# Performance work log

Measured on AMD Instinct MI355X. Metric: run time of the kernel, lower is better.

Reference implementation:

```python
import jax, jax.numpy as jnp
import numpy as np

RADIUS = 0.2
NSAMPLE = 32

B, N, S, C = 4, 16384, 4096, 64


def _ball_query(xyz, new_xyz):
    """CUDA ball_query semantics: for each centroid, the first NSAMPLE point
    indices with squared distance < radius^2 (in index order); empty slots are
    filled with the first found index (0 if no neighbor).
    xyz: [B,N,3], new_xyz: [B,S,3] -> idx [B,S,NSAMPLE] int32."""
    n = xyz.shape[1]
    # squared pairwise distances [B,S,N] via |a|^2 + |b|^2 - 2 a.b
    d2 = (jnp.sum(new_xyz * new_xyz, -1)[:, :, None]
          + jnp.sum(xyz * xyz, -1)[:, None, :]
          - 2.0 * jnp.einsum('bsd,bnd->bsn', new_xyz, xyz))
    in_ball = d2 < RADIUS * RADIUS
    # key = point index if in ball else N (sentinel); sorting gives first-K order
    key = jnp.where(in_ball, jnp.arange(n, dtype=jnp.int32), jnp.int32(n))
    key = jnp.sort(key, axis=-1)[..., :NSAMPLE]          # [B,S,K]
    first = key[..., :1]
    first = jnp.where(first == n, 0, first)              # no neighbor -> 0
    idx = jnp.where(key == n, first, key)
    return idx


def _group(feat, idx):
    """feat [B,C,N], idx [B,S,K] -> [B,C,S,K] (group_points_forward)."""
    return jax.vmap(lambda f, i: f[:, i])(feat, idx)


def setup_inputs() -> dict:
    key = jax.random.key(0)
    k1, k2, k3 = jax.random.split(key, 3)
    xyz = jax.random.uniform(k1, (B, N, 3), dtype=jnp.float32)
    new_xyz = jax.random.uniform(k2, (B, S, 3), dtype=jnp.float32)
    features = jax.random.normal(k3, (B, C, N), dtype=jnp.float32)
    return {"xyz": xyz, "new_xyz": new_xyz, "features": features}


def reference(xyz, new_xyz, features):
    idx = jax.lax.stop_gradient(_ball_query(xyz, new_xyz))   # [B,S,K], non-diff
    xyz_t = jnp.transpose(xyz, (0, 2, 1))                    # [B,3,N]
    grouped_xyz = _group(xyz_t, idx)                         # [B,3,S,K]
    grouped_xyz = grouped_xyz - jnp.transpose(new_xyz, (0, 2, 1))[..., None]
    grouped_features = _group(features, idx)                 # [B,C,S,K]
    new_features = jnp.concatenate([grouped_xyz, grouped_features], axis=1)
    return new_features                                      # [B,3+C,S,K]
```

## Files before the change

### kernel.cpp

```cpp
#include <hip/hip_runtime.h>
#include <stdint.h>

#define BB 4
#define NN 16384
#define SS 4096
#define CC 64
#define KK 32

#define T_INT    10736108
#define LOW_INT  10709108
#define BAND_W   54000

#define PACKED_BYTES ((size_t)BB * NN * sizeof(float4))
#define IDX_BYTES    ((size_t)BB * SS * KK * sizeof(int))

typedef short short2v __attribute__((ext_vector_type(2)));

static __device__ __forceinline__ int mbcnt64(unsigned long long m) {
    return (int)__builtin_amdgcn_mbcnt_hi((unsigned)(m >> 32),
               __builtin_amdgcn_mbcnt_lo((unsigned)m, 0u));
}

#if __has_builtin(__builtin_amdgcn_sdot2)
static __device__ __forceinline__ int dot2i(short2v a, short2v b, int c) {
    return __builtin_amdgcn_sdot2(a, b, c, false);
}
#else
static __device__ __forceinline__ int dot2i(short2v a, short2v b, int c) {
    return (int)a.x * (int)b.x + (int)a.y * (int)b.y + c;
}
#endif

static __device__ __forceinline__ unsigned short f2bf(float f) {
    unsigned u = __builtin_bit_cast(unsigned, f);
    return (unsigned short)((u + 0x7FFFu + ((u >> 16) & 1u)) >> 16);
}
static __device__ __forceinline__ float bf_lo(unsigned w) {
    return __builtin_bit_cast(float, w << 16);
}
static __device__ __forceinline__ float bf_hi(unsigned w) {
    return __builtin_bit_cast(float, w & 0xFFFF0000u);
}

__global__ __launch_bounds__(256) void prep_kernel(const float* __restrict__ xyz,
                                                   const float* __restrict__ features,
                                                   float4* __restrict__ packed,
                                                   ushort4* __restrict__ qpts,
                                                   unsigned short* __restrict__ featB) {
    int blk = blockIdx.x;
    if (blk < 64) {
        for (int i = 0; i < 4; ++i) {
            int p = blk * 1024 + i * 256 + (int)threadIdx.x;
            float x = xyz[(size_t)p * 3 + 0];
            float y = xyz[(size_t)p * 3 + 1];
            float z = xyz[(size_t)p * 3 + 2];
            packed[p] = make_float4(x, y, z, 0.0f);
            ushort4 q;
            q.x = (unsigned short)rintf(x * 16383.0f);
            q.y = (unsigned short)rintf(y * 16383.0f);
            q.z = (unsigned short)rintf(z * 16383.0f);
            q.w = 0;
            qpts[p] = q;
        }
        return;
    }
    blk -= 64;
    int b  = blk >> 8;
    int n0 = (blk & 255) << 6;
    const float* f = features + (size_t)b * CC * NN;
    for (int i = 0; i < 4; ++i) {
        int e  = (int)threadIdx.x + i * 256;
        int c4 = e & 15;
        int n  = n0 + (e >> 4);
        ushort4 v;
        v.x = f2bf(f[(size_t)(c4 * 4 + 0) * NN + n]);
        v.y = f2bf(f[(size_t)(c4 * 4 + 1) * NN + n]);
        v.z = f2bf(f[(size_t)(c4 * 4 + 2) * NN + n]);
        v.w = f2bf(f[(size_t)(c4 * 4 + 3) * NN + n]);
        *(ushort4*)(featB + ((size_t)b * NN + n) * 64 + c4 * 4) = v;
    }
}

__global__ __launch_bounds__(256) void fused_kernel(const float4* __restrict__ packed,
                                                    const ushort4* __restrict__ qpts,
                                                    const float* __restrict__ new_xyz,
                                                    const unsigned short* __restrict__ featB,
                                                    float* __restrict__ out) {
    __shared__ int   sidx[128];
    __shared__ float snc[12];
    __shared__ uint4 sfeat[64][8];

    int bid  = (int)blockIdx.x;
    int wgid = (bid & 7) * 512 + (bid >> 3);
    int b  = wgid >> 10;
    int s0 = (wgid & 1023) << 2;
    int t  = (int)threadIdx.x;
    int w = t >> 6, lane = t & 63;
    int s = s0 + w;

    if (t < 12) snc[t] = new_xyz[((size_t)(b * SS + s0 + t / 3)) * 3 + (t % 3)];

    const float* nc = new_xyz + (size_t)(b * SS + s) * 3;
    const float nxf = nc[0], nyf = nc[1], nzf = nc[2];
    const int qcx = (int)rintf(nxf * 16383.0f);
    const int qcy = (int)rintf(nyf * 16383.0f);
    const int qcz = (int)rintf(nzf * 16383.0f);
    const short2v cxy2 = __builtin_bit_cast(short2v, (unsigned)((qcy << 16) | (qcx & 0xFFFF)));
    const short2v cz2  = __builtin_bit_cast(short2v, (unsigned)qcz);
    const double nx = (double)nxf, ny = (double)nyf, nz = (double)nzf;
    const double t1 = nx * nx + ny * ny + nz * nz;
    const double r2 = 0.2 * 0.2;

    const float4* pts = packed + (size_t)b * NN;
    const uint4*  qv  = (const uint4*)(qpts + (size_t)b * NN);

#define TESTQ(WXY, WZ, J, INB)                                                  \
    {                                                                           \
        short2v dxy = __builtin_bit_cast(short2v, (WXY)) - cxy2;                \
        short2v dz2 = __builtin_bit_cast(short2v, (WZ))  - cz2;                 \
        int d2i = dot2i(dxy, dxy, dot2i(dz2, dz2, 0));                          \
        if ((unsigned)(d2i - LOW_INT) < (unsigned)BAND_W) {                     \
            float4 p = pts[J];                                                  \
            double pxd = (double)p.x, pyd = (double)p.y, pzd = (double)p.z;     \
            double t2d = pxd * pxd + pyd * pyd + pzd * pzd;                     \
            double dtd = nx * pxd + ny * pyd + nz * pzd;                        \
            INB = ((t1 + t2d) - 2.0 * dtd) < r2;                                \
        } else {                                                                \
            INB = d2i < T_INT;                                                  \
        }                                                                       \
    }

    int cnt = 0;
    int first = 0;
    uint4 u0 = qv[lane];
    uint4 u1 = qv[64 + lane];
    for (int i = 0; i < NN / 2; i += 128) {
        int nb = (i + 128 < NN / 2) ? (i + 128) : i;
        uint4 n0 = qv[nb + lane];
        uint4 n1 = qv[nb + 64 + lane];
        int base = i * 2;
        int jA = base + 2 * lane;
        int jC = base + 128 + 2 * lane;

        bool iA, iB, iC, iD;
        TESTQ(u0.x, u0.y, jA, iA)
        TESTQ(u0.z, u0.w, jA + 1, iB)
        TESTQ(u1.x, u1.y, jC, iC)
        TESTQ(u1.z, u1.w, jC + 1, iD)

        unsigned long long mA = __ballot(iA);
        unsigned long long mB = __ballot(iB);
        unsigned long long mC = __ballot(iC);
        unsigned long long mD = __ballot(iD);

        if (cnt == 0 && (mA | mB | mC | mD)) {
            if (mA | mB) {
                int cA = mA ? 2 * (int)__builtin_ctzll(mA)     : 0x7FFFFFFF;
                int cB = mB ? 2 * (int)__builtin_ctzll(mB) + 1 : 0x7FFFFFFF;
                first = base + (cA < cB ? cA : cB);
            } else {
                int cC = mC ? 2 * (int)__builtin_ctzll(mC)     : 0x7FFFFFFF;
                int cD = mD ? 2 * (int)__builtin_ctzll(mD) + 1 : 0x7FFFFFFF;
                first = base + 128 + (cC < cD ? cC : cD);
            }
        }
        int preAB = mbcnt64(mA) + mbcnt64(mB);
        int cAB   = (int)__popcll(mA) + (int)__popcll(mB);
        int preCD = mbcnt64(mC) + mbcnt64(mD);
        if (iA) { int sl = cnt + preAB;                      if (sl < KK) sidx[w * KK + sl] = jA; }
        if (iB) { int sl = cnt + preAB + (iA ? 1 : 0);       if (sl < KK) sidx[w * KK + sl] = jA + 1; }
        if (iC) { int sl = cnt + cAB + preCD;                if (sl < KK) sidx[w * KK + sl] = jC; }
        if (iD) { int sl = cnt + cAB + preCD + (iC ? 1 : 0); if (sl < KK) sidx[w * KK + sl] = jC + 1; }
        cnt += cAB + (int)__popcll(mC) + (int)__popcll(mD);
        if (cnt >= KK) break;
        u0 = n0; u1 = n1;
    }
#undef TESTQ
    if (lane >= cnt && lane < KK) sidx[w * KK + lane] = first;
    __syncthreads();

    const size_t cs = (size_t)SS * KK;
    size_t obase = (size_t)(b * 67) * cs + (size_t)s0 * KK;
    if (t < 128) {
        int cl = t >> 5, k = t & 31;
        float4 p = pts[sidx[t]];
        size_t o = obase + (size_t)cl * KK + k;
        out[o]          = p.x - snc[cl * 3 + 0];
        out[o + cs]     = p.y - snc[cl * 3 + 1];
        out[o + 2 * cs] = p.z - snc[cl * 3 + 2];
    }

    for (int pass = 0; pass < 2; ++pass) {
        {
            int rl = t >> 2;
            int q  = t & 3;
            const uint4* src = (const uint4*)(featB +
                ((size_t)b * NN + sidx[pass * 64 + rl]) * 64);
            sfeat[rl][(q * 2     + rl) & 7] = src[q * 2];
            sfeat[rl][(q * 2 + 1 + rl) & 7] = src[q * 2 + 1];
        }
        __syncthreads();

        float* pbase = out + obase + (size_t)pass * 64;
        for (int cc = 0; cc < 2; ++cc) {
            int c8 = w * 2 + cc;
            uint4 v = sfeat[lane][(c8 + lane) & 7];
            float* pl = pbase + lane;
            size_t cb = (size_t)(3 + c8 * 8) * cs;
            pl[cb]          = bf_lo(v.x);
            pl[cb + cs]     = bf_hi(v.x);
            pl[cb + 2 * cs] = bf_lo(v.y);
            pl[cb + 3 * cs] = bf_hi(v.y);
            pl[cb + 4 * cs] = bf_lo(v.z);
            pl[cb + 5 * cs] = bf_hi(v.z);
            pl[cb + 6 * cs] = bf_lo(v.w);
            pl[cb + 7 * cs] = bf_hi(v.w);
        }
        __syncthreads();
    }
}

extern "C" void kernel_launch(void* const* d_in, const int* in_sizes, int n_in,
                              void* d_out, int out_size, void* d_ws, size_t ws_size,
                              hipStream_t stream) {
    const float* xyz      = (const float*)d_in[0];
    const float* new_xyz  = (const float*)d_in[1];
    const float* features = (const float*)d_in[2];
    float* out = (float*)d_out;

    float4*         packed = (float4*)d_ws;
    ushort4*        qpts   = (ushort4*)((char*)d_ws + PACKED_BYTES);
    unsigned short* featB  = (unsigned short*)((char*)d_ws + PACKED_BYTES + IDX_BYTES);

    prep_kernel<<<64 + BB * (NN / 64), 256, 0, stream>>>(xyz, features, packed,
                                                         qpts, featB);
    fused_kernel<<<BB * SS / 4, 256, 0, stream>>>(packed, qpts, new_xyz, featB, out);
}
```

Baseline: 45.76 us.

## Make gather/scatter phase wave-local to remove block-wide barriers

Each wave now gathers and writes out its own centroid's 32 neighbors, using a per-wave shared-memory slice, instead of the block cooperatively handling all four centroids in two passes. This removes the three __syncthreads barriers and the shared centroid-coordinate staging, so waves that finish the ball query early can start writing without waiting for the rest of the block. In exchange, output stores become 32-float segments per wave rather than 64/128-float contiguous runs, which may reduce write coalescing. The code also relies on wavefront-synchronous access to shared memory with no explicit wave barrier.

```diff
diff --git a/kernel.cpp b/kernel.cpp
--- a/kernel.cpp
+++ b/kernel.cpp
@@ -87,8 +87,7 @@
                                                     const unsigned short* __restrict__ featB,
                                                     float* __restrict__ out) {
     __shared__ int   sidx[128];
-    __shared__ float snc[12];
-    __shared__ uint4 sfeat[64][8];
+    __shared__ uint4 sfeat[4][32][8];
 
     int bid  = (int)blockIdx.x;
     int wgid = (bid & 7) * 512 + (bid >> 3);
@@ -97,8 +96,6 @@
     int t  = (int)threadIdx.x;
     int w = t >> 6, lane = t & 63;
     int s = s0 + w;
-
-    if (t < 12) snc[t] = new_xyz[((size_t)(b * SS + s0 + t / 3)) * 3 + (t % 3)];
 
     const float* nc = new_xyz + (size_t)(b * SS + s) * 3;
     const float nxf = nc[0], nyf = nc[1], nzf = nc[2];
@@ -177,46 +174,42 @@
     }
 #undef TESTQ
     if (lane >= cnt && lane < KK) sidx[w * KK + lane] = first;
-    __syncthreads();
 
     const size_t cs = (size_t)SS * KK;
-    size_t obase = (size_t)(b * 67) * cs + (size_t)s0 * KK;
-    if (t < 128) {
-        int cl = t >> 5, k = t & 31;
-        float4 p = pts[sidx[t]];
-        size_t o = obase + (size_t)cl * KK + k;
-        out[o]          = p.x - snc[cl * 3 + 0];
-        out[o + cs]     = p.y - snc[cl * 3 + 1];
-        out[o + 2 * cs] = p.z - snc[cl * 3 + 2];
-    }
-
-    for (int pass = 0; pass < 2; ++pass) {
-        {
-            int rl = t >> 2;
-            int q  = t & 3;
-            const uint4* src = (const uint4*)(featB +
-                ((size_t)b * NN + sidx[pass * 64 + rl]) * 64);
-            sfeat[rl][(q * 2     + rl) & 7] = src[q * 2];
-            sfeat[rl][(q * 2 + 1 + rl) & 7] = src[q * 2 + 1];
-        }
-        __syncthreads();
-
-        float* pbase = out + obase + (size_t)pass * 64;
-        for (int cc = 0; cc < 2; ++cc) {
-            int c8 = w * 2 + cc;
-            uint4 v = sfeat[lane][(c8 + lane) & 7];
-            float* pl = pbase + lane;
-            size_t cb = (size_t)(3 + c8 * 8) * cs;
-            pl[cb]          = bf_lo(v.x);
-            pl[cb + cs]     = bf_hi(v.x);
-            pl[cb + 2 * cs] = bf_lo(v.y);
-            pl[cb + 3 * cs] = bf_hi(v.y);
-            pl[cb + 4 * cs] = bf_lo(v.z);
-            pl[cb + 5 * cs] = bf_hi(v.z);
-            pl[cb + 6 * cs] = bf_lo(v.w);
-            pl[cb + 7 * cs] = bf_hi(v.w);
-        }
-        __syncthreads();
+    size_t obase = (size_t)(b * 67) * cs + (size_t)s * KK;
+
+    if (lane < KK) {
+        float4 p = pts[sidx[w * KK + lane]];
+        size_t o = obase + lane;
+        out[o]          = p.x - nxf;
+        out[o + cs]     = p.y - nyf;
+        out[o + 2 * cs] = p.z - nzf;
+    }
+
+    {
+        int row = lane >> 1;
+        int q   = lane & 1;
+        const uint4* src = (const uint4*)(featB +
+            ((size_t)b * NN + sidx[w * KK + row]) * 64) + q * 4;
+#pragma unroll
+        for (int j = 0; j < 4; ++j)
+            sfeat[w][row][(q * 4 + j + row) & 7] = src[j];
+    }
+
+#pragma unroll
+    for (int i = 0; i < 4; ++i) {
+        int k  = lane & 31;
+        int c8 = i * 2 + (lane >> 5);
+        uint4 v = sfeat[w][k][(c8 + k) & 7];
+        float* pl = out + obase + (size_t)(3 + c8 * 8) * cs + k;
+        pl[0]               = bf_lo(v.x);
+        pl[cs]              = bf_hi(v.x);
+        pl[2 * cs]          = bf_lo(v.y);
+        pl[3 * cs]          = bf_hi(v.y);
+        pl[4 * cs]          = bf_lo(v.z);
+        pl[5 * cs]          = bf_hi(v.z);
+        pl[6 * cs]          = bf_lo(v.w);
+        pl[7 * cs]          = bf_hi(v.w);
     }
 }
 
```

After: 45.90 us. About the same (+0.3%).

## Process sixteen centroids per block and gather all feature rows in one pass

Applied to the files above, without the earlier changes.

Each workgroup now loops over four groups of four centroids, so the grid shrinks from 4096 to 1024 blocks. The feature gather loads all 128 neighbour rows into a larger shared buffer in a single pass, with four uint4 loads per thread. The two-pass loop and one barrier per group are removed. This is meant to amortise per-block setup and barrier cost, but it cuts the number of resident waves and may reduce latency hiding on the irregular ball-query search.

```diff
diff --git a/kernel.cpp b/kernel.cpp
--- a/kernel.cpp
+++ b/kernel.cpp
@@ -88,37 +88,42 @@
                                                     float* __restrict__ out) {
     __shared__ int   sidx[128];
     __shared__ float snc[12];
-    __shared__ uint4 sfeat[64][8];
+    __shared__ uint4 sfeat[128][8];
 
     int bid  = (int)blockIdx.x;
-    int wgid = (bid & 7) * 512 + (bid >> 3);
-    int b  = wgid >> 10;
-    int s0 = (wgid & 1023) << 2;
+    int wgid = (bid & 7) * 128 + (bid >> 3);
+    int b     = wgid >> 8;
+    int sbase = (wgid & 255) << 4;
     int t  = (int)threadIdx.x;
     int w = t >> 6, lane = t & 63;
-    int s = s0 + w;
-
-    if (t < 12) snc[t] = new_xyz[((size_t)(b * SS + s0 + t / 3)) * 3 + (t % 3)];
-
-    const float* nc = new_xyz + (size_t)(b * SS + s) * 3;
-    const float nxf = nc[0], nyf = nc[1], nzf = nc[2];
-    const int qcx = (int)rintf(nxf * 16383.0f);
-    const int qcy = (int)rintf(nyf * 16383.0f);
-    const int qcz = (int)rintf(nzf * 16383.0f);
-    const short2v cxy2 = __builtin_bit_cast(short2v, (unsigned)((qcy << 16) | (qcx & 0xFFFF)));
-    const short2v cz2  = __builtin_bit_cast(short2v, (unsigned)qcz);
-    const double nx = (double)nxf, ny = (double)nyf, nz = (double)nzf;
-    const double t1 = nx * nx + ny * ny + nz * nz;
-    const double r2 = 0.2 * 0.2;
 
     const float4* pts = packed + (size_t)b * NN;
     const uint4*  qv  = (const uint4*)(qpts + (size_t)b * NN);
+    const size_t cs = (size_t)SS * KK;
+
+    for (int g = 0; g < 4; ++g) {
+        int s0 = sbase + g * 4;
+        int s  = s0 + w;
+
+        if (t < 12) snc[t] = new_xyz[((size_t)(b * SS + s0 + t / 3)) * 3 + (t % 3)];
+
+        const float* nc = new_xyz + (size_t)(b * SS + s) * 3;
+        const float nxf = nc[0], nyf = nc[1], nzf = nc[2];
+        const int qcx = (int)rintf(nxf * 16383.0f);
+        const int qcy = (int)rintf(nyf * 16383.0f);
+        const int qcz = (int)rintf(nzf * 16383.0f);
+        const short2v cxy2 = __builtin_bit_cast(short2v,
+                                (unsigned)((qcy << 16) | (qcx & 0xFFFF)));
+        const short2v cz2  = __builtin_bit_cast(short2v, (unsigned)qcz);
+        const double nx = (double)nxf, ny = (double)nyf, nz = (double)nzf;
+        const double t1 = nx * nx + ny * ny + nz * nz;
+        const double r2 = 0.2 * 0.2;
 
 #define TESTQ(WXY, WZ, J, INB)                                                  \
     {                                                                           \
         short2v dxy = __builtin_bit_cast(short2v, (WXY)) - cxy2;                \
-        short2v dz2 = __builtin_bit_cast(short2v, (WZ))  - cz2;                 \
-        int d2i = dot2i(dxy, dxy, dot2i(dz2, dz2, 0));                          \
+        short2v dzv = __builtin_bit_cast(short2v, (WZ))  - cz2;                 \
+        int d2i = dot2i(dxy, dxy, dot2i(dzv, dzv, 0));                          \
         if ((unsigned)(d2i - LOW_INT) < (unsigned)BAND_W) {                     \
             float4 p = pts[J];                                                  \
             double pxd = (double)p.x, pyd = (double)p.y, pzd = (double)p.z;     \
@@ -130,93 +135,92 @@
         }                                                                       \
     }
 
-    int cnt = 0;
-    int first = 0;
-    uint4 u0 = qv[lane];
-    uint4 u1 = qv[64 + lane];
-    for (int i = 0; i < NN / 2; i += 128) {
-        int nb = (i + 128 < NN / 2) ? (i + 128) : i;
-        uint4 n0 = qv[nb + lane];
-        uint4 n1 = qv[nb + 64 + lane];
-        int base = i * 2;
-        int jA = base + 2 * lane;
-        int jC = base + 128 + 2 * lane;
-
-        bool iA, iB, iC, iD;
-        TESTQ(u0.x, u0.y, jA, iA)
-        TESTQ(u0.z, u0.w, jA + 1, iB)
-        TESTQ(u1.x, u1.y, jC, iC)
-        TESTQ(u1.z, u1.w, jC + 1, iD)
-
-        unsigned long long mA = __ballot(iA);
-        unsigned long long mB = __ballot(iB);
-        unsigned long long mC = __ballot(iC);
-        unsigned long long mD = __ballot(iD);
-
-        if (cnt == 0 && (mA | mB | mC | mD)) {
-            if (mA | mB) {
-                int cA = mA ? 2 * (int)__builtin_ctzll(mA)     : 0x7FFFFFFF;
-                int cB = mB ? 2 * (int)__builtin_ctzll(mB) + 1 : 0x7FFFFFFF;
-                first = base + (cA < cB ? cA : cB);
-            } else {
-                int cC = mC ? 2 * (int)__builtin_ctzll(mC)     : 0x7FFFFFFF;
-                int cD = mD ? 2 * (int)__builtin_ctzll(mD) + 1 : 0x7FFFFFFF;
-                first = base + 128 + (cC < cD ? cC : cD);
+        int cnt = 0;
+        int first = 0;
+        uint4 u0 = qv[lane];
+        uint4 u1 = qv[64 + lane];
+        for (int i = 0; i < NN / 2; i += 128) {
+            int nb = (i + 128 < NN / 2) ? (i + 128) : i;
+            uint4 p0q = qv[nb + lane];
+            uint4 p1q = qv[nb + 64 + lane];
+            int base = i * 2;
+            int jA = base + 2 * lane;
+            int jC = base + 128 + 2 * lane;
+
+            bool iA, iB, iC, iD;
+            TESTQ(u0.x, u0.y, jA, iA)
+            TESTQ(u0.z, u0.w, jA + 1, iB)
+            TESTQ(u1.x, u1.y, jC, iC)
+            TESTQ(u1.z, u1.w, jC + 1, iD)
+
+            unsigned long long mA = __ballot(iA);
+            unsigned long long mB = __ballot(iB);
+            unsigned long long mC = __ballot(iC);
+            unsigned long long mD = __ballot(iD);
+
+            if (cnt == 0 && (mA | mB | mC | mD)) {
+                if (mA | mB) {
+                    int cA = mA ? 2 * (int)__builtin_ctzll(mA)     : 0x7FFFFFFF;
+                    int cB = mB ? 2 * (int)__builtin_ctzll(mB) + 1 : 0x7FFFFFFF;
+                    first = base + (cA < cB ? cA : cB);
+                } else {
+                    int cC = mC ? 2 * (int)__builtin_ctzll(mC)     : 0x7FFFFFFF;
+                    int cD = mD ? 2 * (int)__builtin_ctzll(mD) + 1 : 0x7FFFFFFF;
+                    first = base + 128 + (cC < cD ? cC : cD);
+                }
             }
-        }
-        int preAB = mbcnt64(mA) + mbcnt64(mB);
-        int cAB   = (int)__popcll(mA) + (int)__popcll(mB);
-        int preCD = mbcnt64(mC) + mbcnt64(mD);
-        if (iA) { int sl = cnt + preAB;                      if (sl < KK) sidx[w * KK + sl] = jA; }
-        if (iB) { int sl = cnt + preAB + (iA ? 1 : 0);       if (sl < KK) sidx[w * KK + sl] = jA + 1; }
-        if (iC) { int sl = cnt + cAB + preCD;                if (sl < KK) sidx[w * KK + sl] = jC; }
-        if (iD) { int sl = cnt + cAB + preCD + (iC ? 1 : 0); if (sl < KK) sidx[w * KK + sl] = jC + 1; }
-        cnt += cAB + (int)__popcll(mC) + (int)__popcll(mD);
-        if (cnt >= KK) break;
-        u0 = n0; u1 = n1;
-    }
+            int preAB = mbcnt64(mA) + mbcnt64(mB);
+            int cAB   = (int)__popcll(mA) + (int)__popcll(mB);
+            int preCD = mbcnt64(mC) + mbcnt64(mD);
+            if (iA) { int sl = cnt + preAB;                      if (sl < KK) sidx[w * KK + sl] = jA; }
+            if (iB) { int sl = cnt + preAB + (iA ? 1 : 0);       if (sl < KK) sidx[w * KK + sl] = jA + 1; }
+            if (iC) { int sl = cnt + cAB + preCD;                if (sl < KK) sidx[w * KK + sl] = jC; }
+            if (iD) { int sl = cnt + cAB + preCD + (iC ? 1 : 0); if (sl < KK) sidx[w * KK + sl] = jC + 1; }
+            cnt += cAB + (int)__popcll(mC) + (int)__popcll(mD);
+            if (cnt >= KK) break;
+            u0 = p0q; u1 = p1q;
+        }
 #undef TESTQ
-    if (lane >= cnt && lane < KK) sidx[w * KK + lane] = first;
-    __syncthreads();
-
-    const size_t cs = (size_t)SS * KK;
-    size_t obase = (size_t)(b * 67) * cs + (size_t)s0 * KK;
-    if (t < 128) {
-        int cl = t >> 5, k = t & 31;
-        float4 p = pts[sidx[t]];
-        size_t o = obase + (size_t)cl * KK + k;
-        out[o]          = p.x - snc[cl * 3 + 0];
-        out[o + cs]     = p.y - snc[cl * 3 + 1];
-        out[o + 2 * cs] = p.z - snc[cl * 3 + 2];
-    }
-
-    for (int pass = 0; pass < 2; ++pass) {
+        if (lane >= cnt && lane < KK) sidx[w * KK + lane] = first;
+        __syncthreads();
+
+        size_t obase = (size_t)(b * 67) * cs + (size_t)s0 * KK;
+
+        if (t < 128) {
+            int cl = t >> 5, k = t & 31;
+            float4 p = pts[sidx[t]];
+            size_t o = obase + (size_t)cl * KK + k;
+            out[o]          = p.x - snc[cl * 3 + 0];
+            out[o + cs]     = p.y - snc[cl * 3 + 1];
+            out[o + 2 * cs] = p.z - snc[cl * 3 + 2];
+        }
         {
-            int rl = t >> 2;
-            int q  = t & 3;
+            int row = t >> 1;
+            int q   = t & 1;
             const uint4* src = (const uint4*)(featB +
-                ((size_t)b * NN + sidx[pass * 64 + rl]) * 64);
-            sfeat[rl][(q * 2     + rl) & 7] = src[q * 2];
-            sfeat[rl][(q * 2 + 1 + rl) & 7] = src[q * 2 + 1];
+                ((size_t)b * NN + sidx[row]) * 64) + q * 4;
+#pragma unroll
+            for (int j = 0; j < 4; ++j)
+                sfeat[row][(q * 4 + j + row) & 7] = src[j];
         }
         __syncthreads();
 
-        float* pbase = out + obase + (size_t)pass * 64;
+#pragma unroll
         for (int cc = 0; cc < 2; ++cc) {
             int c8 = w * 2 + cc;
-            uint4 v = sfeat[lane][(c8 + lane) & 7];
-            float* pl = pbase + lane;
-            size_t cb = (size_t)(3 + c8 * 8) * cs;
-            pl[cb]          = bf_lo(v.x);
-            pl[cb + cs]     = bf_hi(v.x);
-            pl[cb + 2 * cs] = bf_lo(v.y);
-            pl[cb + 3 * cs] = bf_hi(v.y);
-            pl[cb + 4 * cs] = bf_lo(v.z);
-            pl[cb + 5 * cs] = bf_hi(v.z);
-            pl[cb + 6 * cs] = bf_lo(v.w);
-            pl[cb + 7 * cs] = bf_hi(v.w);
-        }
-        __syncthreads();
+            int col = (c8 + lane) & 7;
+            uint4 v0 = sfeat[lane][col];
+            uint4 v1 = sfeat[64 + lane][col];
+            float* pl = out + obase + (size_t)(3 + c8 * 8) * cs + lane;
+            pl[0]           = bf_lo(v0.x);  pl[64]          = bf_lo(v1.x);
+            pl[cs]          = bf_hi(v0.x);  pl[cs + 64]     = bf_hi(v1.x);
+            pl[2 * cs]      = bf_lo(v0.y);  pl[2 * cs + 64] = bf_lo(v1.y);
+            pl[3 * cs]      = bf_hi(v0.y);  pl[3 * cs + 64] = bf_hi(v1.y);
+            pl[4 * cs]      = bf_lo(v0.z);  pl[4 * cs + 64] = bf_lo(v1.z);
+            pl[5 * cs]      = bf_hi(v0.z);  pl[5 * cs + 64] = bf_hi(v1.z);
+            pl[6 * cs]      = bf_lo(v0.w);  pl[6 * cs + 64] = bf_lo(v1.w);
+            pl[7 * cs]      = bf_hi(v0.w);  pl[7 * cs + 64] = bf_hi(v1.w);
+        }
     }
 }
 
@@ -234,5 +238,5 @@
 
     prep_kernel<<<64 + BB * (NN / 64), 256, 0, stream>>>(xyz, features, packed,
                                                          qpts, featB);
-    fused_kernel<<<BB * SS / 4, 256, 0, stream>>>(packed, qpts, new_xyz, featB, out);
-}
+    fused_kernel<<<BB * SS / 16, 256, 0, stream>>>(packed, qpts, new_xyz, featB, out);
+}
```

Measured after the change: 54.98 us. 1.2x slower.
